# Performance work log

Hardware: AMD Instinct MI355X
Metric: run time of the kernel (lower is better)

Reference implementation:

```python
import jax, jax.numpy as jnp
import numpy as np
import math

B, NLAT, DIM = 16, 64, 768
DEPTH, HEADS, DH = 6, 16, 64
INNER = HEADS * DH          # 1024
FF = 4 * DIM                # 3072
FR_DIMS = [64, 128, 256, 512]
LENS = [3136, 784, 196, 49]  # 56^2, 28^2, 14^2, 7^2 backbone stages
EPS = 1e-5


def layernorm(x, w, b):
    m = jnp.mean(x, axis=-1, keepdims=True)
    v = jnp.mean((x - m) ** 2, axis=-1, keepdims=True)
    return (x - m) * jax.lax.rsqrt(v + EPS) * w + b


def perceiver_attn(x, latents, ln1w, ln1b, ln2w, ln2b, wq, wkv, wo):
    # x: (b, n1, D) image features; latents: (b, n2, D)
    xn = layernorm(x, ln1w, ln1b)
    ln_lat = layernorm(latents, ln2w, ln2b)
    b, l, _ = ln_lat.shape
    q = ln_lat @ wq                                   # (b, n2, H*Dh)
    kv = jnp.concatenate([xn, ln_lat], axis=1) @ wkv  # (b, n1+n2, 2*H*Dh)
    k, v = jnp.split(kv, 2, axis=-1)
    def to_heads(t):
        return t.reshape(b, t.shape[1], HEADS, DH).transpose(0, 2, 1, 3)
    q, k, v = to_heads(q), to_heads(k), to_heads(v)   # (b, h, n, Dh)
    scale = 1.0 / math.sqrt(math.sqrt(DH))            # double-sqrt scaling
    w = jnp.einsum('bhqd,bhkd->bhqk', q * scale, k * scale)
    w = jax.nn.softmax(w.astype(jnp.float32), axis=-1).astype(q.dtype)
    out = jnp.einsum('bhqk,bhkd->bhqd', w, v)
    out = out.transpose(0, 2, 1, 3).reshape(b, l, INNER)
    return out @ wo


def setup_inputs() -> dict:
    key = jax.random.key(0)
    ks = iter(jax.random.split(key, 48))
    nrm = lambda shape, s=0.02: (jax.random.normal(next(ks), shape, jnp.float32) * s)
    inp = {
        'id_embedding': jax.random.normal(next(ks), (B, NLAT, DIM), jnp.float32),
        'f0': jax.random.normal(next(ks), (B, LENS[0], FR_DIMS[0]), jnp.float32),
        'f1': jax.random.normal(next(ks), (B, LENS[1], FR_DIMS[1]), jnp.float32),
        'f2': jax.random.normal(next(ks), (B, LENS[2], FR_DIMS[2]), jnp.float32),
        'f3': jax.random.normal(next(ks), (B, LENS[3], FR_DIMS[3]), jnp.float32),
        # per-scale input projections (Linear with bias)
        'p0_w': nrm((FR_DIMS[0], DIM)), 'p0_b': jnp.zeros((DIM,), jnp.float32),
        'p1_w': nrm((FR_DIMS[1], DIM)), 'p1_b': jnp.zeros((DIM,), jnp.float32),
        'p2_w': nrm((FR_DIMS[2], DIM)), 'p2_b': jnp.zeros((DIM,), jnp.float32),
        'p3_w': nrm((FR_DIMS[3], DIM)), 'p3_b': jnp.zeros((DIM,), jnp.float32),
        # stacked PerceiverAttention params: (depth, 4 scales, ...)
        'attn_ln1_w': jnp.ones((DEPTH, 4, DIM), jnp.float32),
        'attn_ln1_b': jnp.zeros((DEPTH, 4, DIM), jnp.float32),
        'attn_ln2_w': jnp.ones((DEPTH, 4, DIM), jnp.float32),
        'attn_ln2_b': jnp.zeros((DEPTH, 4, DIM), jnp.float32),
        'attn_wq': nrm((DEPTH, 4, DIM, INNER)),
        'attn_wkv': nrm((DEPTH, 4, DIM, 2 * INNER)),
        'attn_wo': nrm((DEPTH, 4, INNER, DIM)),
        # stacked FeedForward params: (depth, ...)
        'ff_ln_w': jnp.ones((DEPTH, DIM), jnp.float32),
        'ff_ln_b': jnp.zeros((DEPTH, DIM), jnp.float32),
        'ff_w1': nrm((DEPTH, DIM, FF)),
        'ff_w2': nrm((DEPTH, FF, DIM)),
        # output head (zero-init in source; randomized here for a nontrivial baseline)
        'proj_out_w': nrm((DIM, DIM)),
        'proj_out_b': jnp.zeros((DIM,), jnp.float32),
        'norm_out_w': jnp.ones((DIM,), jnp.float32),
        'norm_out_b': jnp.zeros((DIM,), jnp.float32),
    }
    return inp


def reference(id_embedding, f0, f1, f2, f3,
              p0_w, p0_b, p1_w, p1_b, p2_w, p2_b, p3_w, p3_b,
              attn_ln1_w, attn_ln1_b, attn_ln2_w, attn_ln2_b,
              attn_wq, attn_wkv, attn_wo,
              ff_ln_w, ff_ln_b, ff_w1, ff_w2,
              proj_out_w, proj_out_b, norm_out_w, norm_out_b):
    # source projects in reversed order: feats[0] <- deepest stage (f3)
    feats = [f3 @ p3_w + p3_b,
             f2 @ p2_w + p2_b,
             f1 @ p1_w + p1_b,
             f0 @ p0_w + p0_b]
    lat = id_embedding
    for d in range(DEPTH):
        for i in range(4):
            lat = perceiver_attn(feats[i], lat,
                                 attn_ln1_w[d, i], attn_ln1_b[d, i],
                                 attn_ln2_w[d, i], attn_ln2_b[d, i],
                                 attn_wq[d, i], attn_wkv[d, i], attn_wo[d, i]) + lat
        h = layernorm(lat, ff_ln_w[d], ff_ln_b[d])
        lat = jax.nn.gelu(h @ ff_w1[d], approximate=False) @ ff_w2[d] + lat
    out = lat @ proj_out_w + proj_out_b
    return layernorm(out, norm_out_w, norm_out_b)
```

## Files before the change

### kernel.cpp

```cpp
#include <hip/hip_runtime.h>
#include <hip/hip_bf16.h>
#include <cstdint>
#include <cstddef>

typedef __hip_bfloat16 bf16;
typedef float  f32x4   __attribute__((ext_vector_type(4)));
typedef float  float4v __attribute__((ext_vector_type(4)));
typedef short  short8  __attribute__((ext_vector_type(8)));
typedef short  short4v __attribute__((ext_vector_type(4)));
typedef __bf16 bf16x8  __attribute__((ext_vector_type(8)));

__device__ __forceinline__ void mfma16(f32x4& d, short8 a, short8 b) {
  d = __builtin_amdgcn_mfma_f32_16x16x32_bf16(
      __builtin_bit_cast(bf16x8, a), __builtin_bit_cast(bf16x8, b), d, 0, 0, 0);
}
__device__ __forceinline__ unsigned short f2b_bits(float x) {
  __hip_bfloat16 h = __float2bfloat16(x);
  return __builtin_bit_cast(unsigned short, h);
}
__device__ __forceinline__ float gelu_exact(float x) {
  return 0.5f * x * (1.0f + erff(x * 0.7071067811865475f));
}

__global__ __launch_bounds__(256) void k_cvt(const float* __restrict__ src,
                                             bf16* __restrict__ dst, int n4) {
  int i = blockIdx.x * 256 + threadIdx.x;
  if (i >= n4) return;
  float4v v = *(const float4v*)(src + (size_t)i * 4);
  short4v s;
  s[0] = (short)f2b_bits(v[0]); s[1] = (short)f2b_bits(v[1]);
  s[2] = (short)f2b_bits(v[2]); s[3] = (short)f2b_bits(v[3]);
  *(short4v*)((short*)dst + (size_t)i * 4) = s;
}

template <bool DUAL>
__global__ __launch_bounds__(256) void k_tfoldx(const float* __restrict__ src,
                                                const float* __restrict__ s1,
                                                const float* __restrict__ s2,
                                                bf16* __restrict__ d1,
                                                bf16* __restrict__ d2,
                                                int K, int N,
                                                long long src_bs, long long s_bs,
                                                long long d1_bs, long long d2_bs) {
  src += (size_t)blockIdx.z * src_bs;
  d1  += (size_t)blockIdx.z * d1_bs;
  if (DUAL) d2 += (size_t)blockIdx.z * d2_bs;
  __shared__ float tile[64][65];
  __shared__ float sc1[64], sc2[64];
  const int n0 = blockIdx.x * 64, k0 = blockIdx.y * 64;
  const int t = threadIdx.x;
  if (t < 64) {
    sc1[t] = s1 ? (s1 + (size_t)blockIdx.z * s_bs)[k0 + t] : 1.0f;
  } else if (DUAL && t < 128) {
    sc2[t - 64] = (s2 + (size_t)blockIdx.z * s_bs)[k0 + t - 64];
  }
#pragma unroll
  for (int j = 0; j < 4; ++j) {
    int f = t + j * 256;
    int row = f >> 4, col = (f & 15) * 4;
    float4v v = *(const float4v*)(src + (size_t)(k0 + row) * N + n0 + col);
    tile[row][col]     = v[0];
    tile[row][col + 1] = v[1];
    tile[row][col + 2] = v[2];
    tile[row][col + 3] = v[3];
  }
  __syncthreads();
#pragma unroll
  for (int j = 0; j < 2; ++j) {
    int s = t + j * 256;
    int n = s >> 3, kc = (s & 7) * 8;
    short8 o1v, o2v;
#pragma unroll
    for (int i = 0; i < 8; ++i) {
      float v = tile[kc + i][n];
      o1v[i] = (short)f2b_bits(v * sc1[kc + i]);
      if (DUAL) o2v[i] = (short)f2b_bits(v * sc2[kc + i]);
    }
    *(short8*)(d1 + (size_t)(n0 + n) * K + k0 + kc) = o1v;
    if (DUAL) *(short8*)(d2 + (size_t)(n0 + n) * K + k0 + kc) = o2v;
  }
}

__global__ __launch_bounds__(256) void k_bfoldv(const float* __restrict__ W,
                                                const float* __restrict__ lnb,
                                                float* __restrict__ out, int K, int N,
                                                long long w_bs, long long b_bs, long long o_bs) {
  W   += (size_t)blockIdx.y * w_bs;
  lnb += (size_t)blockIdx.y * b_bs;
  out += (size_t)blockIdx.y * o_bs;
  __shared__ float sb[768];
  for (int k = threadIdx.x; k < K; k += 256) sb[k] = lnb[k];
  __syncthreads();
  const int lane = threadIdx.x & 63, kg = threadIdx.x >> 6;
  const int n = blockIdx.x * 256 + lane * 4;
  float4v a = {0.f, 0.f, 0.f, 0.f};
  for (int k = kg; k < K; k += 4) {
    float4v wv = *(const float4v*)(W + (size_t)k * N + n);
    float c = sb[k];
    a[0] = fmaf(c, wv[0], a[0]); a[1] = fmaf(c, wv[1], a[1]);
    a[2] = fmaf(c, wv[2], a[2]); a[3] = fmaf(c, wv[3], a[3]);
  }
  __shared__ float4v red[4][64];
  red[kg][lane] = a;
  __syncthreads();
  if (kg == 0) {
    float4v r = red[0][lane] + red[1][lane] + red[2][lane] + red[3][lane];
    *(float4v*)(out + n) = r;
  }
}

__global__ __launch_bounds__(256) void k_kvfold(const float* __restrict__ wkv,
                                                const float* __restrict__ ln2b,
                                                const float* __restrict__ ln1b,
                                                const float* __restrict__ ln1w,
                                                const float* __restrict__ b0,
                                                const float* __restrict__ b1,
                                                const float* __restrict__ b2,
                                                const float* __restrict__ b3,
                                                float* __restrict__ pbuf) {
  const int di = blockIdx.y;
  const int kz = blockIdx.z;
  const int i = di & 3;
  const float* pb = (i == 0) ? b0 : (i == 1) ? b1 : (i == 2) ? b2 : b3;
  const float* W = wkv + (size_t)di * 768 * 2048;
  __shared__ float c2b[96], c1b[96], c1w[96], cpw[96];
  if (threadIdx.x < 96) {
    int k = kz * 96 + threadIdx.x;
    float w1 = ln1w[(size_t)di * 768 + k];
    c2b[threadIdx.x] = ln2b[(size_t)di * 768 + k];
    c1b[threadIdx.x] = ln1b[(size_t)di * 768 + k];
    c1w[threadIdx.x] = w1;
    cpw[threadIdx.x] = pb[k] * w1;
  }
  __syncthreads();
  const int lane = threadIdx.x & 63, kg = threadIdx.x >> 6;
  const int n = blockIdx.x * 256 + lane * 4;
  float4v a1 = {0.f,0.f,0.f,0.f}, a2 = a1, a3 = a1, a4 = a1;
  for (int kk = kg; kk < 96; kk += 4) {
    float4v wv = *(const float4v*)(W + (size_t)(kz * 96 + kk) * 2048 + n);
    float s1 = c2b[kk], s2 = c1b[kk], s3 = c1w[kk], s4 = cpw[kk];
#pragma unroll
    for (int q = 0; q < 4; ++q) {
      a1[q] = fmaf(s1, wv[q], a1[q]);
      a2[q] = fmaf(s2, wv[q], a2[q]);
      a3[q] = fmaf(s3, wv[q], a3[q]);
      a4[q] = fmaf(s4, wv[q], a4[q]);
    }
  }
  __shared__ float4v red[4][64];
  red[kg][lane] = a1; __syncthreads();
  if (kg == 0) {
    float4v r = red[0][lane] + red[1][lane] + red[2][lane] + red[3][lane];
    *(float4v*)(pbuf + (((size_t)0 * 8 + kz) * 24 + di) * 2048 + n) = r;
  }
  __syncthreads();
  red[kg][lane] = a2; __syncthreads();
  if (kg == 0) {
    float4v r = red[0][lane] + red[1][lane] + red[2][lane] + red[3][lane];
    *(float4v*)(pbuf + (((size_t)1 * 8 + kz) * 24 + di) * 2048 + n) = r;
  }
  __syncthreads();
  red[kg][lane] = a3; __syncthreads();
  if (kg == 0) {
    float4v r = red[0][lane] + red[1][lane] + red[2][lane] + red[3][lane];
    *(float4v*)(pbuf + (((size_t)2 * 8 + kz) * 24 + di) * 2048 + n) = r;
  }
  __syncthreads();
  red[kg][lane] = a4; __syncthreads();
  if (kg == 0) {
    float4v r = red[0][lane] + red[1][lane] + red[2][lane] + red[3][lane];
    *(float4v*)(pbuf + (((size_t)3 * 8 + kz) * 24 + di) * 2048 + n) = r;
  }
}

__global__ __launch_bounds__(256) void k_kvred(const float* __restrict__ pbuf,
                                               float* __restrict__ qb,
                                               float* __restrict__ kb,
                                               float* __restrict__ sv,
                                               float* __restrict__ bw) {
  const int di = blockIdx.y;
  const int n = blockIdx.x * 256 + threadIdx.x;
  float a0 = 0.f, a1 = 0.f, a2 = 0.f, a3 = 0.f;
  for (int kz = 0; kz < 8; ++kz) {
    a0 += pbuf[(((size_t)0 * 8 + kz) * 24 + di) * 2048 + n];
    a1 += pbuf[(((size_t)1 * 8 + kz) * 24 + di) * 2048 + n];
    a2 += pbuf[(((size_t)2 * 8 + kz) * 24 + di) * 2048 + n];
    a3 += pbuf[(((size_t)3 * 8 + kz) * 24 + di) * 2048 + n];
  }
  qb[(size_t)di * 3072 + 1024 + n] = a0;
  kb[(size_t)di * 2048 + n] = a1;
  sv[(size_t)di * 2048 + n] = a2;
  bw[(size_t)di * 2048 + n] = a3;
}

__global__ __launch_bounds__(256) void k_std(const float* __restrict__ src,
                                             bf16* __restrict__ dst) {
  int row = blockIdx.x;
  const float* x = src + (size_t)row * 768;
  int t = threadIdx.x;
  float a0 = x[t], a1 = x[t + 256], a2 = x[t + 512];
  float s = a0 + a1 + a2;
  float q = a0 * a0 + a1 * a1 + a2 * a2;
#pragma unroll
  for (int off = 1; off < 64; off <<= 1) { s += __shfl_xor(s, off); q += __shfl_xor(q, off); }
  __shared__ float ss[4], qs[4];
  if ((t & 63) == 0) { ss[t >> 6] = s; qs[t >> 6] = q; }
  __syncthreads();
  s = ss[0] + ss[1] + ss[2] + ss[3];
  q = qs[0] + qs[1] + qs[2] + qs[3];
  float mean = s * (1.0f / 768.0f);
  float var  = q * (1.0f / 768.0f) - mean * mean;
  float inv  = rsqrtf(var + 1e-5f);
  bf16* d = dst + (size_t)row * 768;
  d[t]       = __float2bfloat16((a0 - mean) * inv);
  d[t + 256] = __float2bfloat16((a1 - mean) * inv);
  d[t + 512] = __float2bfloat16((a2 - mean) * inv);
}

__global__ __launch_bounds__(256) void k_stats(const float* __restrict__ src,
                                               float2* __restrict__ out) {
  int row = blockIdx.x;
  const float* x = src + (size_t)row * 768;
  int t = threadIdx.x;
  float a0 = x[t], a1 = x[t + 256], a2 = x[t + 512];
  float s = a0 + a1 + a2;
  float q = a0 * a0 + a1 * a1 + a2 * a2;
#pragma unroll
  for (int off = 1; off < 64; off <<= 1) { s += __shfl_xor(s, off); q += __shfl_xor(q, off); }
  __shared__ float ss[4], qs[4];
  if ((t & 63) == 0) { ss[t >> 6] = s; qs[t >> 6] = q; }
  __syncthreads();
  if (t == 0) {
    float sm = ss[0] + ss[1] + ss[2] + ss[3];
    float qm = qs[0] + qs[1] + qs[2] + qs[3];
    float mean = sm * (1.0f / 768.0f);
    float var  = qm * (1.0f / 768.0f) - mean * mean;
    float inv  = rsqrtf(var + 1e-5f);
    out[row] = make_float2(inv, mean * inv);
  }
}

__global__ __launch_bounds__(256) void k_lnout(const float* __restrict__ src,
                                               const float* __restrict__ w,
                                               const float* __restrict__ b,
                                               float* __restrict__ dst) {
  int row = blockIdx.x;
  const float* x = src + (size_t)row * 768;
  int t = threadIdx.x;
  float a0 = x[t], a1 = x[t + 256], a2 = x[t + 512];
  float s = a0 + a1 + a2;
  float q = a0 * a0 + a1 * a1 + a2 * a2;
#pragma unroll
  for (int off = 1; off < 64; off <<= 1) { s += __shfl_xor(s, off); q += __shfl_xor(q, off); }
  __shared__ float ss[4], qs[4];
  if ((t & 63) == 0) { ss[t >> 6] = s; qs[t >> 6] = q; }
  __syncthreads();
  s = ss[0] + ss[1] + ss[2] + ss[3];
  q = qs[0] + qs[1] + qs[2] + qs[3];
  float mean = s * (1.0f / 768.0f);
  float var  = q * (1.0f / 768.0f) - mean * mean;
  float inv  = rsqrtf(var + 1e-5f);
  float* d = dst + (size_t)row * 768;
  d[t]       = (a0 - mean) * inv * w[t]       + b[t];
  d[t + 256] = (a1 - mean) * inv * w[t + 256] + b[t + 256];
  d[t + 512] = (a2 - mean) * inv * w[t + 512] + b[t + 512];
}

template <int BM, int BN, bool OBF16, bool GELU, bool KVE>
__global__ __launch_bounds__(256) void k_gemm(const bf16* __restrict__ A,
                                              const bf16* __restrict__ Bt,
                                              void* __restrict__ Cv,
                                              const float* __restrict__ bias,
                                              const float* __restrict__ res,
                                              const float2* __restrict__ rstats,
                                              const float* __restrict__ c1,
                                              const float* __restrict__ cs,
                                              int M, int N, int K, int nxt, int nwg) {
  constexpr int AI = BM / 32, BI = BN / 32;
  constexpr int MF = BM / 32, NF = BN / 32;
  __shared__ __align__(16) char smem[(BM + BN) * 128];
  char* As = smem;
  char* Bs = smem + BM * 128;

  const int lin = blockIdx.x;
  const int qq = nwg >> 3, r8 = nwg & 7;
  const int xcd = lin & 7, idx = lin >> 3;
  const int swz = (xcd < r8) ? (xcd * (qq + 1) + idx)
                             : (r8 * (qq + 1) + (xcd - r8) * qq + idx);
  const int bm = (swz / nxt) * BM, bn = (swz % nxt) * BN;

  const int t = threadIdx.x, lane = t & 63, w = t >> 6;
  const int wr = w >> 1, wc = w & 1;
  const int l15 = lane & 15, lg = lane >> 4;
  const int srow = t >> 3, scol = t & 7;

  const bf16* aptr[AI]; int aoff[AI];
#pragma unroll
  for (int i = 0; i < AI; ++i) {
    int r = i * 32 + srow;
    int gr = bm + r; if (gr > M - 1) gr = M - 1;
    aptr[i] = A + (size_t)gr * K + scol * 8;
    aoff[i] = r * 128 + ((scol * 16) ^ ((r & 7) << 4));
  }
  const bf16* bptr[BI]; int boff[BI];
#pragma unroll
  for (int i = 0; i < BI; ++i) {
    int r = i * 32 + srow;
    int gc = bn + r; if (gc > N - 1) gc = N - 1;
    bptr[i] = Bt + (size_t)gc * K + scol * 8;
    boff[i] = r * 128 + ((scol * 16) ^ ((r & 7) << 4));
  }

  f32x4 acc[MF][NF] = {};
  short8 av[AI], bv[BI];
#pragma unroll
  for (int i = 0; i < AI; ++i) av[i] = *(const short8*)(aptr[i]);
#pragma unroll
  for (int i = 0; i < BI; ++i) bv[i] = *(const short8*)(bptr[i]);

  const int nk = K / 64;
  for (int kt = 0; kt < nk; ++kt) {
    __syncthreads();
#pragma unroll
    for (int i = 0; i < AI; ++i) *(short8*)(As + aoff[i]) = av[i];
#pragma unroll
    for (int i = 0; i < BI; ++i) *(short8*)(Bs + boff[i]) = bv[i];
    __syncthreads();
    if (kt + 1 < nk) {
#pragma unroll
      for (int i = 0; i < AI; ++i) av[i] = *(const short8*)(aptr[i] + (size_t)(kt + 1) * 64);
#pragma unroll
      for (int i = 0; i < BI; ++i) bv[i] = *(const short8*)(bptr[i] + (size_t)(kt + 1) * 64);
    }
#pragma unroll
    for (int ks = 0; ks < 2; ++ks) {
      short8 af[MF], bfr[NF];
#pragma unroll
      for (int m = 0; m < MF; ++m) {
        int r = wr * (BM / 2) + m * 16 + l15;
        af[m] = *(const short8*)(As + r * 128 + ((ks * 64 + lg * 16) ^ ((r & 7) << 4)));
      }
#pragma unroll
      for (int n = 0; n < NF; ++n) {
        int r = wc * (BN / 2) + n * 16 + l15;
        bfr[n] = *(const short8*)(Bs + r * 128 + ((ks * 64 + lg * 16) ^ ((r & 7) << 4)));
      }
#pragma unroll
      for (int m = 0; m < MF; ++m)
#pragma unroll
        for (int n = 0; n < NF; ++n) mfma16(acc[m][n], af[m], bfr[n]);
    }
  }

  if (OBF16) {
    __syncthreads();
    bf16* cst = (bf16*)smem;
#pragma unroll
    for (int m = 0; m < MF; ++m) {
      int lr0 = wr * (BM / 2) + m * 16 + lg * 4;
#pragma unroll
      for (int n = 0; n < NF; ++n) {
        int lc = wc * (BN / 2) + n * 16 + l15;
        int gc = bn + lc;
        float bvs = bias ? bias[gc] : 0.0f;
        float c1v = 0.0f, csv = 0.0f;
        if (KVE) { c1v = c1[gc]; csv = cs[gc]; }
#pragma unroll
        for (int r = 0; r < 4; ++r) {
          int row = lr0 + r;
          float v;
          if (KVE) {
            int gri = bm + row; if (gri > M - 1) gri = M - 1;
            float2 st = rstats[gri];
            v = (acc[m][n][r] + c1v) * st.x - st.y * csv + bvs;
          } else {
            v = acc[m][n][r] + bvs;
            if (GELU) v = gelu_exact(v);
          }
          cst[row * BN + lc] = __float2bfloat16(v);
        }
      }
    }
    __syncthreads();
    constexpr int CB = BN / 8;
    constexpr int SEGS = BM * CB;
    for (int seg = t; seg < SEGS; seg += 256) {
      int row = seg / CB, cb = seg % CB;
      int gr = bm + row;
      if (gr < M)
        *(short8*)((bf16*)Cv + (size_t)gr * N + bn + cb * 8) =
            *(const short8*)(cst + (size_t)row * BN + cb * 8);
    }
  } else {
#pragma unroll
    for (int m = 0; m < MF; ++m) {
      int gr0 = bm + wr * (BM / 2) + m * 16 + lg * 4;
#pragma unroll
      for (int n = 0; n < NF; ++n) {
        int gc = bn + wc * (BN / 2) + n * 16 + l15;
        float bvs = bias ? bias[gc] : 0.0f;
#pragma unroll
        for (int r = 0; r < 4; ++r) {
          int gr = gr0 + r;
          if (gr < M) {
            float v = acc[m][n][r] + bvs;
            if (GELU) v = gelu_exact(v);
            if (res) v += res[(size_t)gr * N + gc];
            ((float*)Cv)[(size_t)gr * N + gc] = v;
          }
        }
      }
    }
  }
}

template <bool FUSED>
__global__ __launch_bounds__(256) void k_attn(const bf16* __restrict__ qkvl,
                                              const bf16* __restrict__ kvx,
                                              bf16* __restrict__ outp,
                                              float* __restrict__ opart,
                                              float* __restrict__ mlpart,
                                              int n1, int b0, int nseg, int nbloc,
                                              const bf16* __restrict__ fsrc,
                                              const bf16* __restrict__ PT,
                                              const float2* __restrict__ rst,
                                              const float* __restrict__ c1vec,
                                              const float* __restrict__ csvec,
                                              const float* __restrict__ lbvec) {
  const int s   = blockIdx.x % nseg;
  const int bh  = blockIdx.x / nseg;
  const int bl = bh >> 4, h = bh & 15;
  const int b = b0 + bl;
  const int nb64 = nbloc * 64;
  __shared__ __align__(16) char Qs[64 * 128];
  __shared__ __align__(16) char Ks[64 * 128];
  __shared__ __align__(16) char Vt[64 * 128];
  __shared__ __align__(16) char Ps[4][16 * 128];
  __shared__ __align__(16) char Fs[FUSED ? 64 * 128 : 16];
  __shared__ __align__(16) char PTks[FUSED ? 64 * 128 : 16];
  __shared__ __align__(16) char PTvs[FUSED ? 64 * 128 : 16];
  __shared__ float2 Rs[FUSED ? 64 : 1];
  const int t = threadIdx.x, lane = t & 63, w = t >> 6;
  const int l15 = lane & 15, lg = lane >> 4;

#pragma unroll
  for (int it = 0; it < 2; ++it) {
    int slot = it * 256 + t; int r = slot >> 3, c = slot & 7;
    short8 v = *(const short8*)(qkvl + (size_t)(b * 64 + r) * 3072 + h * 64 + c * 8);
    *(short8*)(Qs + r * 128 + ((c * 16) ^ ((r & 7) << 4))) = v;
  }
  float c1k[4], csk[4], lbk[4], c1v_[4], csv_[4], lbv_[4];
  if constexpr (FUSED) {
#pragma unroll
    for (int it = 0; it < 2; ++it) {
      int slot = it * 256 + t; int r = slot >> 3, c = slot & 7;
      *(short8*)(PTks + r * 128 + ((c * 16) ^ ((r & 7) << 4))) =
          *(const short8*)(PT + (size_t)(h * 64 + r) * 64 + c * 8);
      *(short8*)(PTvs + r * 128 + ((c * 16) ^ ((r & 7) << 4))) =
          *(const short8*)(PT + (size_t)(1024 + h * 64 + r) * 64 + c * 8);
    }
#pragma unroll
    for (int n = 0; n < 4; ++n) {
      int dk = h * 64 + n * 16 + l15;
      c1k[n] = c1vec[dk]; csk[n] = csvec[dk]; lbk[n] = lbvec[dk];
      int dv = 1024 + dk;
      c1v_[n] = c1vec[dv]; csv_[n] = csvec[dv]; lbv_[n] = lbvec[dv];
    }
  }
  const int n_kv = n1 + 64;
  const int nch = (n_kv + 63) >> 6;
  const int cpseg = (nch + nseg - 1) / nseg;
  const int ch0 = s * cpseg;
  const int ch1 = min(nch, ch0 + cpseg);

  float m_run = -1e30f, l_run = 0.0f;
  f32x4 o[4] = {};

  short8 kreg[2], vreg[2], freg[2];
  float2 rreg = make_float2(0.f, 0.f);
  auto loadKV = [&](int ch) {
#pragma unroll
    for (int it = 0; it < 2; ++it) {
      int slot = it * 256 + t; int rr = slot >> 3, c = slot & 7;
      int j = ch * 64 + rr;
      short8 kv = {}; short8 vv = {};
      if (j < n_kv) {
        const bf16* kb;
        if (j < n1) kb = kvx + (size_t)(bl * n1 + j) * 2048 + h * 64;
        else        kb = qkvl + (size_t)(b * 64 + (j - n1)) * 3072 + 1024 + h * 64;
        kv = *(const short8*)(kb + c * 8);
        vv = *(const short8*)(kb + 1024 + c * 8);
      }
      kreg[it] = kv; vreg[it] = vv;
    }
  };
  auto loadF = [&](int ch) {
#pragma unroll
    for (int it = 0; it < 2; ++it) {
      int slot = it * 256 + t; int rr = slot >> 3, c = slot & 7;
      freg[it] = *(const short8*)(fsrc + ((size_t)b * n1 + (size_t)ch * 64 + rr) * 64 + c * 8);
    }
    if (t < 64) rreg = rst[(size_t)b * n1 + (size_t)ch * 64 + t];
  };
  auto isLat = [&](int ch) { return ch * 64 >= n1; };

  if (FUSED && !isLat(ch0)) loadF(ch0); else loadKV(ch0);

  for (int ch = ch0; ch < ch1; ++ch) {
    const bool lat = !FUSED || isLat(ch);
    __syncthreads();
    if (lat) {
#pragma unroll
      for (int it = 0; it < 2; ++it) {
        int slot = it * 256 + t; int rr = slot >> 3, c = slot & 7;
        *(short8*)(Ks + rr * 128 + ((c * 16) ^ ((rr & 7) << 4))) = kreg[it];
#pragma unroll
        for (int j2 = 0; j2 < 8; ++j2) {
          int dh = c * 8 + j2;
          *(short*)(Vt + dh * 128 + ((rr * 2) ^ ((dh & 7) << 4))) = vreg[it][j2];
        }
      }
    } else {
#pragma unroll
      for (int it = 0; it < 2; ++it) {
        int slot = it * 256 + t; int rr = slot >> 3, c = slot & 7;
        *(short8*)(Fs + rr * 128 + ((c * 16) ^ ((rr & 7) << 4))) = freg[it];
      }
      if (t < 64) Rs[t] = rreg;
    }
    __syncthreads();
    if (ch + 1 < ch1) {
      if (FUSED && !isLat(ch + 1)) loadF(ch + 1); else loadKV(ch + 1);
    }
    if constexpr (FUSED) {
      if (!lat) {
        f32x4 ka[4] = {};
#pragma unroll
        for (int ks = 0; ks < 2; ++ks) {
          int fr = w * 16 + l15;
          short8 ff = *(const short8*)(Fs + fr * 128 + ((ks * 64 + lg * 16) ^ ((fr & 7) << 4)));
#pragma unroll
          for (int n = 0; n < 4; ++n) {
            int pr = n * 16 + l15;
            short8 pk = *(const short8*)(PTks + pr * 128 + ((ks * 64 + lg * 16) ^ ((pr & 7) << 4)));
            mfma16(ka[n], ff, pk);
          }
        }
#pragma unroll
        for (int n = 0; n < 4; ++n)
#pragma unroll
          for (int r = 0; r < 4; ++r) {
            int jl = w * 16 + lg * 4 + r;
            float2 st = Rs[jl];
            float v = (ka[n][r] + c1k[n]) * st.x - st.y * csk[n] + lbk[n];
            int dh = n * 16 + l15;
            *(unsigned short*)(Ks + jl * 128 + ((dh * 2) ^ ((jl & 7) << 4))) = f2b_bits(v);
          }
        f32x4 va[4] = {};
#pragma unroll
        for (int ks = 0; ks < 2; ++ks) {
          int fr = w * 16 + l15;
          short8 ff = *(const short8*)(Fs + fr * 128 + ((ks * 64 + lg * 16) ^ ((fr & 7) << 4)));
#pragma unroll
          for (int n = 0; n < 4; ++n) {
            int pr = n * 16 + l15;
            short8 pv = *(const short8*)(PTvs + pr * 128 + ((ks * 64 + lg * 16) ^ ((pr & 7) << 4)));
            mfma16(va[n], ff, pv);
          }
        }
#pragma unroll
        for (int n = 0; n < 4; ++n)
#pragma unroll
          for (int r = 0; r < 4; ++r) {
            int jl = w * 16 + lg * 4 + r;
            float2 st = Rs[jl];
            float v = (va[n][r] + c1v_[n]) * st.x - st.y * csv_[n] + lbv_[n];
            int dh = n * 16 + l15;
            *(unsigned short*)(Vt + dh * 128 + ((jl * 2) ^ ((dh & 7) << 4))) = f2b_bits(v);
          }
      }
      __syncthreads();
    }

    f32x4 sc[4] = {};
#pragma unroll
    for (int ks = 0; ks < 2; ++ks) {
      int qr = w * 16 + l15;
      short8 qf = *(const short8*)(Qs + qr * 128 + ((ks * 64 + lg * 16) ^ ((qr & 7) << 4)));
#pragma unroll
      for (int n = 0; n < 4; ++n) {
        int kr = n * 16 + l15;
        short8 kf = *(const short8*)(Ks + kr * 128 + ((ks * 64 + lg * 16) ^ ((kr & 7) << 4)));
        mfma16(sc[n], kf, qf);
      }
    }
    float mx = m_run;
#pragma unroll
    for (int n = 0; n < 4; ++n)
#pragma unroll
      for (int r = 0; r < 4; ++r) {
        float v = sc[n][r] * 0.125f;
        int kvi = ch * 64 + n * 16 + lg * 4 + r;
        if (kvi >= n_kv) v = -1e30f;
        sc[n][r] = v;
        mx = fmaxf(mx, v);
      }
    mx = fmaxf(mx, __shfl_xor(mx, 16));
    mx = fmaxf(mx, __shfl_xor(mx, 32));
    float scl = __expf(m_run - mx);
    m_run = mx;
    float p[4][4];
    float rs = 0.0f;
#pragma unroll
    for (int n = 0; n < 4; ++n)
#pragma unroll
      for (int r = 0; r < 4; ++r) { float pv = __expf(sc[n][r] - mx); p[n][r] = pv; rs += pv; }
    rs += __shfl_xor(rs, 16);
    rs += __shfl_xor(rs, 32);
    l_run = l_run * scl + rs;
    float sclq[4];
#pragma unroll
    for (int r = 0; r < 4; ++r) sclq[r] = __shfl(scl, lg * 4 + r);
#pragma unroll
    for (int nn = 0; nn < 4; ++nn)
#pragma unroll
      for (int r = 0; r < 4; ++r) o[nn][r] *= sclq[r];
#pragma unroll
    for (int n = 0; n < 4; ++n)
#pragma unroll
      for (int r = 0; r < 4; ++r) {
        int kv = n * 16 + lg * 4 + r;
        *(unsigned short*)(Ps[w] + l15 * 128 + ((kv * 2) ^ ((l15 & 7) << 4))) = f2b_bits(p[n][r]);
      }
#pragma unroll
    for (int ks = 0; ks < 2; ++ks) {
      short8 pf = *(const short8*)(Ps[w] + l15 * 128 + ((ks * 64 + lg * 16) ^ ((l15 & 7) << 4)));
#pragma unroll
      for (int nn = 0; nn < 4; ++nn) {
        int dh = nn * 16 + l15;
        short8 vf = *(const short8*)(Vt + dh * 128 + ((ks * 64 + lg * 16) ^ ((dh & 7) << 4)));
        mfma16(o[nn], pf, vf);
      }
    }
  }

  if (nseg == 1) {
    float lq[4];
#pragma unroll
    for (int r = 0; r < 4; ++r) lq[r] = __shfl(l_run, lg * 4 + r);
#pragma unroll
    for (int nn = 0; nn < 4; ++nn)
#pragma unroll
      for (int r = 0; r < 4; ++r) {
        int qr = w * 16 + lg * 4 + r;
        int dh = nn * 16 + l15;
        outp[(size_t)(b * 64 + qr) * 1024 + h * 64 + dh] = __float2bfloat16(o[nn][r] / lq[r]);
      }
  } else {
#pragma unroll
    for (int nn = 0; nn < 4; ++nn)
#pragma unroll
      for (int r = 0; r < 4; ++r) {
        int qr = w * 16 + lg * 4 + r;
        int dh = nn * 16 + l15;
        opart[((size_t)s * nb64 + bl * 64 + qr) * 1024 + h * 64 + dh] = o[nn][r];
      }
    if (lg == 0) {
      int qr = w * 16 + l15;
      size_t mi = (((size_t)s * nb64 + bl * 64 + qr) * 16 + h) * 2;
      mlpart[mi]     = m_run;
      mlpart[mi + 1] = l_run;
    }
  }
}

__global__ __launch_bounds__(256) void k_amerge(const float* __restrict__ opart,
                                                const float* __restrict__ mlpart,
                                                bf16* __restrict__ outp,
                                                int b0, int nseg, int nbloc) {
  const int bh = blockIdx.x;
  const int bl = bh >> 4, h = bh & 15;
  const int nb64 = nbloc * 64;
  const int t = threadIdx.x;
  const int q = t >> 2, quarter = t & 3;

  float ms[8], ls[8];
  float mstar = -1e30f;
  for (int s = 0; s < nseg; ++s) {
    size_t mi = (((size_t)s * nb64 + bl * 64 + q) * 16 + h) * 2;
    ms[s] = mlpart[mi]; ls[s] = mlpart[mi + 1];
    mstar = fmaxf(mstar, ms[s]);
  }
  float L = 0.0f, ws[8];
  for (int s = 0; s < nseg; ++s) { ws[s] = __expf(ms[s] - mstar); L += ws[s] * ls[s]; }
  float inv = 1.0f / L;

  bf16* outrow = outp + (size_t)((b0 + bl) * 64 + q) * 1024 + h * 64;
#pragma unroll
  for (int jj = 0; jj < 4; ++jj) {
    int dh0 = quarter * 16 + jj * 4;
    float4v acc = {0.f, 0.f, 0.f, 0.f};
    for (int s = 0; s < nseg; ++s) {
      const float* orow = opart + ((size_t)s * nb64 + bl * 64 + q) * 1024 + h * 64 + dh0;
      float4v v = *(const float4v*)orow;
      acc[0] += ws[s] * v[0]; acc[1] += ws[s] * v[1];
      acc[2] += ws[s] * v[2]; acc[3] += ws[s] * v[3];
    }
    short4v sv;
    sv[0] = (short)f2b_bits(acc[0] * inv); sv[1] = (short)f2b_bits(acc[1] * inv);
    sv[2] = (short)f2b_bits(acc[2] * inv); sv[3] = (short)f2b_bits(acc[3] * inv);
    *(short4v*)((short*)(outrow + dh0)) = sv;
  }
}

extern "C" void kernel_launch(void* const* d_in, const int* in_sizes, int n_in,
                              void* d_out, int out_size, void* d_ws, size_t ws_size,
                              hipStream_t stream) {
  (void)in_sizes; (void)n_in; (void)out_size;
  const float* id_emb = (const float*)d_in[0];
  const float* f_in[4]  = {(const float*)d_in[4],  (const float*)d_in[3],
                           (const float*)d_in[2],  (const float*)d_in[1]};
  const float* pw_in[4] = {(const float*)d_in[11], (const float*)d_in[9],
                           (const float*)d_in[7],  (const float*)d_in[5]};
  const float* pb_in[4] = {(const float*)d_in[12], (const float*)d_in[10],
                           (const float*)d_in[8],  (const float*)d_in[6]};
  const float* ln1w = (const float*)d_in[13];
  const float* ln1b = (const float*)d_in[14];
  const float* ln2w = (const float*)d_in[15];
  const float* ln2b = (const float*)d_in[16];
  const float* wq   = (const float*)d_in[17];
  const float* wkv  = (const float*)d_in[18];
  const float* wo   = (const float*)d_in[19];
  const float* fflnw = (const float*)d_in[20];
  const float* fflnb = (const float*)d_in[21];
  const float* ffw1  = (const float*)d_in[22];
  const float* ffw2  = (const float*)d_in[23];
  const float* projw = (const float*)d_in[24];
  const float* projb = (const float*)d_in[25];
  const float* normw = (const float*)d_in[26];
  const float* normb = (const float*)d_in[27];

  static const int N1S[4]  = {49, 196, 784, 3136};
  static const int FRDS[4] = {512, 256, 128, 64};
  static const int NSEG[4] = {1, 1, 2, 4};
  const size_t LW = 4718592;
  static const size_t ROFF[4] = {0, 16*49ull, 16*(49+196ull), 16*(49+196+784ull)};

  bf16 *fbf[4], *pT[4], *pbf[4], *projT, *PTbuf;
  float *qkvl_bias, *kvx_bias, *ff_bias, *lat, *headtmp, *svv, *bwv, *pbuf;
  float2 *rstats;
  float *opart, *mlpart;
  bf16 *qkvl_act, *attnout, *zlat, *latbf, *ffh;
  bf16 *wqkvlT = nullptr, *wkvxT = nullptr, *woT = nullptr, *w1T = nullptr, *w2T = nullptr;
  bf16 *wbuf = nullptr;
  char *big;

  auto assign = [&](bool fullw, int bc) -> size_t {
    size_t off = 0; char* base = (char*)d_ws;
    auto A = [&](size_t b) -> char* {
      char* p = base + off; off = (off + b + 255) & ~(size_t)255; return p;
    };
    for (int i = 0; i < 4; ++i) fbf[i] = (bf16*)A((size_t)16 * N1S[i] * FRDS[i] * 2);
    for (int i = 0; i < 4; ++i) pT[i]  = (bf16*)A((size_t)768 * FRDS[i] * 2);
    for (int i = 0; i < 4; ++i) pbf[i] = (bf16*)A((size_t)FRDS[i] * 768 * 2);
    projT     = (bf16*)A(768ull * 768 * 2);
    PTbuf     = (bf16*)A(2048ull * 512 * 2);
    qkvl_bias = (float*)A(24ull * 3072 * 4);
    kvx_bias  = (float*)A(24ull * 2048 * 4);
    ff_bias   = (float*)A(6ull * 3072 * 4);
    svv       = (float*)A(24ull * 2048 * 4);
    bwv       = (float*)A(24ull * 2048 * 4);
    pbuf      = (float*)A(4ull * 8 * 24 * 2048 * 4);
    rstats    = (float2*)A(16ull * 4165 * 8);
    qkvl_act  = (bf16*)A(1024ull * 3072 * 2);
    attnout   = (bf16*)A(1024ull * 1024 * 2);
    lat       = (float*)A(1024ull * 768 * 4);
    zlat      = (bf16*)A(1024ull * 768 * 2);
    opart     = (float*)A(4ull * (size_t)bc * 64 * 1024 * 4);
    mlpart    = (float*)A(4ull * (size_t)bc * 64 * 16 * 2 * 4);
    if (fullw) {
      wqkvlT = (bf16*)A(24ull * 3072 * 768 * 2);
      wkvxT  = (bf16*)A(24ull * 2048 * 768 * 2);
      woT    = (bf16*)A(24ull * 768 * 1024 * 2);
      w1T    = (bf16*)A(6ull * 3072 * 768 * 2);
      w2T    = (bf16*)A(6ull * 768 * 3072 * 2);
      wbuf = nullptr;
    } else {
      wbuf = (bf16*)A(4ull * LW * 2);
      wqkvlT = wkvxT = woT = w1T = w2T = nullptr;
    }
    big = A((size_t)bc * 3136 * 2048 * 2);
    ffh = qkvl_act; headtmp = (float*)qkvl_act; latbf = zlat;
    return off;
  };

  static const bool FULLS[10] = {true,true,false,true,false,true,true,false,false,false};
  static const int  BCS[10]   = {16,  8,   16,   4,   8,    2,   1,   4,    2,    1};
  bool fullw = false; int bc = 1; bool ok = false;
  for (int c = 0; c < 10; ++c) {
    if (assign(FULLS[c], BCS[c]) <= ws_size) { fullw = FULLS[c]; bc = BCS[c]; ok = true; break; }
  }
  if (!ok) return;

  float* featf32 = (float*)big;
  bf16*  kvxbuf  = (bf16*)big;

  auto gemm = [&](int tile, const bf16* A, const bf16* Bt, void* C,
                  const float* bias, const float* res, int M, int N, int K,
                  bool obf, bool gl) {
    if (tile == 128) {
      int nxt = N / 128, nwg = nxt * ((M + 127) / 128);
      if (obf && gl) k_gemm<128,128,true ,true ,false><<<nwg,256,0,stream>>>(A,Bt,C,bias,res,nullptr,nullptr,nullptr,M,N,K,nxt,nwg);
      else if (obf)  k_gemm<128,128,true ,false,false><<<nwg,256,0,stream>>>(A,Bt,C,bias,res,nullptr,nullptr,nullptr,M,N,K,nxt,nwg);
      else           k_gemm<128,128,false,false,false><<<nwg,256,0,stream>>>(A,Bt,C,bias,res,nullptr,nullptr,nullptr,M,N,K,nxt,nwg);
    } else if (tile == 64) {
      int nxt = N / 64, nwg = nxt * ((M + 63) / 64);
      if (obf && gl)  k_gemm<64,64,true ,true ,false><<<nwg,256,0,stream>>>(A,Bt,C,bias,res,nullptr,nullptr,nullptr,M,N,K,nxt,nwg);
      else if (obf)   k_gemm<64,64,true ,false,false><<<nwg,256,0,stream>>>(A,Bt,C,bias,res,nullptr,nullptr,nullptr,M,N,K,nxt,nwg);
      else            k_gemm<64,64,false,false,false><<<nwg,256,0,stream>>>(A,Bt,C,bias,res,nullptr,nullptr,nullptr,M,N,K,nxt,nwg);
    } else {
      int nxt = N / 64, nwg = nxt * ((M + 31) / 32);
      if (obf && gl)  k_gemm<32,64,true ,true ,false><<<nwg,256,0,stream>>>(A,Bt,C,bias,res,nullptr,nullptr,nullptr,M,N,K,nxt,nwg);
      else if (obf)   k_gemm<32,64,true ,false,false><<<nwg,256,0,stream>>>(A,Bt,C,bias,res,nullptr,nullptr,nullptr,M,N,K,nxt,nwg);
      else            k_gemm<32,64,false,false,false><<<nwg,256,0,stream>>>(A,Bt,C,bias,res,nullptr,nullptr,nullptr,M,N,K,nxt,nwg);
    }
  };
  auto gemmkv = [&](const bf16* A, const bf16* Bt, void* C,
                    const float* lb, const float2* rst, const float* c1, const float* cs,
                    int M, int N, int K) {
    if (M >= 2048) {
      int nxt = N / 128, nwg = nxt * ((M + 127) / 128);
      k_gemm<128,128,true,false,true><<<nwg,256,0,stream>>>(A,Bt,C,lb,nullptr,rst,c1,cs,M,N,K,nxt,nwg);
    } else {
      int nxt = N / 64, nwg = nxt * ((M + 63) / 64);
      k_gemm<64,64,true,false,true><<<nwg,256,0,stream>>>(A,Bt,C,lb,nullptr,rst,c1,cs,M,N,K,nxt,nwg);
    }
  };
  auto pick = [&](int M, int N) -> int {
    return M >= 2048 ? 128 : (N >= 1536 ? 64 : 32);
  };

  k_bfoldv<<<dim3(4, 24), 256, 0, stream>>>(wq,  ln2b, qkvl_bias, 768, 1024, 768LL*1024, 768, 3072);
  k_kvfold<<<dim3(8, 24, 8), 256, 0, stream>>>(wkv, ln2b, ln1b, ln1w,
                                               pb_in[0], pb_in[1], pb_in[2], pb_in[3], pbuf);
  k_kvred<<<dim3(8, 24), 256, 0, stream>>>(pbuf, qkvl_bias, kvx_bias, svv, bwv);
  k_bfoldv<<<dim3(12, 6), 256, 0, stream>>>(ffw1, fflnb, ff_bias, 768, 3072, 768LL*3072, 768, 3072);

  for (int i = 0; i < 4; ++i) {
    k_tfoldx<false><<<dim3(12, FRDS[i] / 64, 1), 256, 0, stream>>>(
        pw_in[i], nullptr, nullptr, pT[i], nullptr, FRDS[i], 768, 0, 0, 0, 0);
    int cnt = FRDS[i] * 768;
    k_cvt<<<cnt / 1024, 256, 0, stream>>>(pw_in[i], pbf[i], cnt / 4);
  }
  k_tfoldx<false><<<dim3(12, 12, 1), 256, 0, stream>>>(
      projw, nullptr, nullptr, projT, nullptr, 768, 768, 0, 0, 0, 0);

  if (fullw) {
    k_tfoldx<false><<<dim3(16, 12, 24), 256, 0, stream>>>(
        wq, ln2w, nullptr, wqkvlT, nullptr, 768, 1024, 768LL*1024, 768, 3072LL*768, 0);
    k_tfoldx<true><<<dim3(32, 12, 24), 256, 0, stream>>>(
        wkv, ln2w, ln1w, wqkvlT + 1024LL*768, wkvxT, 768, 2048,
        768LL*2048, 768, 3072LL*768, 2048LL*768);
    k_tfoldx<false><<<dim3(12, 16, 24), 256, 0, stream>>>(
        wo, nullptr, nullptr, woT, nullptr, 1024, 768, 1024LL*768, 0, 768LL*1024, 0);
    k_tfoldx<false><<<dim3(48, 12, 6), 256, 0, stream>>>(
        ffw1, fflnw, nullptr, w1T, nullptr, 768, 3072, 768LL*3072, 768, 3072LL*768, 0);
    k_tfoldx<false><<<dim3(12, 48, 6), 256, 0, stream>>>(
        ffw2, nullptr, nullptr, w2T, nullptr, 3072, 768, 3072LL*768, 0, 768LL*3072, 0);
  }

  auto foldDepthAttn = [&](int d) {
    k_tfoldx<false><<<dim3(16, 12, 4), 256, 0, stream>>>(
        wq + (size_t)d*4*768*1024, ln2w + (size_t)d*4*768, nullptr,
        wbuf, nullptr, 768, 1024, 768LL*1024, 768, (long long)LW, 0);
    k_tfoldx<true><<<dim3(32, 12, 4), 256, 0, stream>>>(
        wkv + (size_t)d*4*768*2048, ln2w + (size_t)d*4*768, ln1w + (size_t)d*4*768,
        wbuf + 1024ull*768, wbuf + 3072ull*768, 768, 2048,
        768LL*2048, 768, (long long)LW, (long long)LW);
    k_tfoldx<false><<<dim3(12, 16, 4), 256, 0, stream>>>(
        wo + (size_t)d*4*1024*768, nullptr, nullptr,
        wbuf + 3932160ull, nullptr, 1024, 768, 1024LL*768, 0, (long long)LW, 0);
  };
  auto attnW = [&](int di, const bf16*& qkvlT_p, const bf16*& kvxT_p, const bf16*& woT_p) {
    if (fullw) {
      qkvlT_p = wqkvlT + (size_t)di * 3072 * 768;
      kvxT_p  = wkvxT  + (size_t)di * 2048 * 768;
      woT_p   = woT    + (size_t)di * 768 * 1024;
    } else {
      bf16* base = wbuf + (size_t)(di & 3) * LW;
      qkvlT_p = base;
      kvxT_p  = base + 2359296ull;
      woT_p   = base + 3932160ull;
    }
  };
  auto ffW = [&](int d, const bf16*& w1p, const bf16*& w2p) {
    if (fullw) {
      w1p = w1T + (size_t)d * 3072 * 768;
      w2p = w2T + (size_t)d * 768 * 3072;
    } else {
      bf16* d1 = wbuf;
      bf16* d2 = wbuf + 3072ull * 768;
      k_tfoldx<false><<<dim3(48, 12, 1), 256, 0, stream>>>(
          ffw1 + (size_t)d*768*3072, fflnw + 768ull*d, nullptr, d1, nullptr,
          768, 3072, 0, 0, 0, 0);
      k_tfoldx<false><<<dim3(12, 48, 1), 256, 0, stream>>>(
          ffw2 + (size_t)d*3072*768, nullptr, nullptr, d2, nullptr,
          3072, 768, 0, 0, 0, 0);
      w1p = d1; w2p = d2;
    }
  };

  for (int i = 0; i < 4; ++i) {
    int n1 = N1S[i], frd = FRDS[i];
    size_t cnt = (size_t)16 * n1 * frd;
    k_cvt<<<(int)(cnt / 1024), 256, 0, stream>>>(f_in[i], fbf[i], (int)(cnt / 4));
    for (int b0 = 0; b0 < 16; b0 += bc) {
      int rows = bc * n1;
      gemm(pick(rows, 768), fbf[i] + (size_t)b0 * n1 * frd, pT[i], featf32,
           pb_in[i], nullptr, rows, 768, frd, false, false);
      k_stats<<<rows, 256, 0, stream>>>(featf32, rstats + ROFF[i] + (size_t)b0 * n1);
    }
  }

  hipMemcpyAsync(lat, id_emb, 1024ull * 768 * 4, hipMemcpyDeviceToDevice, stream);

  for (int d = 0; d < 6; ++d) {
    if (!fullw) foldDepthAttn(d);
    for (int i = 0; i < 4; ++i) {
      int di = d * 4 + i, n1 = N1S[i], nseg = NSEG[i], frd = FRDS[i];
      const bf16 *qkvlT_p, *kvxT_p, *woT_p;
      attnW(di, qkvlT_p, kvxT_p, woT_p);
      gemm(64, kvxT_p, pbf[i], PTbuf, nullptr, nullptr, 2048, frd, 768, true, false);
      k_std<<<1024, 256, 0, stream>>>(lat, zlat);
      gemm(64, zlat, qkvlT_p, qkvl_act, qkvl_bias + 3072ull * di, nullptr,
           1024, 3072, 768, true, false);
      for (int b0 = 0; b0 < 16; b0 += bc) {
        int rows = bc * n1;
        if (i == 3) {
          k_attn<true><<<bc * 16 * nseg, 256, 0, stream>>>(
              qkvl_act, kvxbuf, attnout, opart, mlpart, n1, b0, nseg, bc,
              fbf[3], PTbuf, rstats + ROFF[3],
              bwv + 2048ull * di, svv + 2048ull * di, kvx_bias + 2048ull * di);
        } else {
          gemmkv(fbf[i] + (size_t)b0 * n1 * frd, PTbuf, kvxbuf,
                 kvx_bias + 2048ull * di, rstats + ROFF[i] + (size_t)b0 * n1,
                 bwv + 2048ull * di, svv + 2048ull * di, rows, 2048, frd);
          k_attn<false><<<bc * 16 * nseg, 256, 0, stream>>>(
              qkvl_act, kvxbuf, attnout, opart, mlpart, n1, b0, nseg, bc,
              nullptr, nullptr, nullptr, nullptr, nullptr, nullptr);
        }
        if (nseg > 1)
          k_amerge<<<bc * 16, 256, 0, stream>>>(opart, mlpart, attnout, b0, nseg, bc);
      }
      gemm(32, attnout, woT_p, lat, nullptr, lat, 1024, 768, 1024, false, false);
    }
    const bf16 *w1p, *w2p;
    ffW(d, w1p, w2p);
    k_std<<<1024, 256, 0, stream>>>(lat, zlat);
    gemm(64, zlat, w1p, ffh, ff_bias + 3072ull * d, nullptr, 1024, 3072, 768, true, true);
    gemm(32, ffh, w2p, lat, nullptr, lat, 1024, 768, 3072, false, false);
  }

  k_cvt<<<768, 256, 0, stream>>>(lat, latbf, 196608);
  gemm(32, latbf, projT, headtmp, projb, nullptr, 1024, 768, 768, false, false);
  k_lnout<<<1024, 256, 0, stream>>>(headtmp, normw, normb, (float*)d_out);
}
```

Measured before the change: 2.951 ms.

## Batch composed KV-projection weight GEMMs upfront and split-K the bias folds

All 24 per-layer products of the KV weight with the input projection weights are now computed before the depth loop. Each scale gets one launch batched over depth through a new blockIdx.y stride in the GEMM kernel, replacing 24 small serialized GEMMs inside the loop. The bias-fold kernels are split along K across 8 z-blocks with a separate reduction kernel, giving more parallelism to what was a tiny grid. This adds workspace for the precomputed products and one extra small launch per bias fold.

```diff
diff --git a/kernel.cpp b/kernel.cpp
--- a/kernel.cpp
+++ b/kernel.cpp
@@ -81,22 +81,22 @@
   }
 }
 
-__global__ __launch_bounds__(256) void k_bfoldv(const float* __restrict__ W,
-                                                const float* __restrict__ lnb,
-                                                float* __restrict__ out, int K, int N,
-                                                long long w_bs, long long b_bs, long long o_bs) {
-  W   += (size_t)blockIdx.y * w_bs;
-  lnb += (size_t)blockIdx.y * b_bs;
-  out += (size_t)blockIdx.y * o_bs;
-  __shared__ float sb[768];
-  for (int k = threadIdx.x; k < K; k += 256) sb[k] = lnb[k];
+__global__ __launch_bounds__(256) void k_bfoldz(const float* __restrict__ W,
+                                                const float* __restrict__ b,
+                                                float* __restrict__ pbuf, int K, int N,
+                                                long long w_bs, long long b_bs) {
+  W += (size_t)blockIdx.y * w_bs;
+  b += (size_t)blockIdx.y * b_bs;
+  const int kz = blockIdx.z, kpz = K >> 3;
+  __shared__ float sb[96];
+  if ((int)threadIdx.x < kpz) sb[threadIdx.x] = b[kz * kpz + threadIdx.x];
   __syncthreads();
   const int lane = threadIdx.x & 63, kg = threadIdx.x >> 6;
   const int n = blockIdx.x * 256 + lane * 4;
   float4v a = {0.f, 0.f, 0.f, 0.f};
-  for (int k = kg; k < K; k += 4) {
-    float4v wv = *(const float4v*)(W + (size_t)k * N + n);
-    float c = sb[k];
+  for (int kk = kg; kk < kpz; kk += 4) {
+    float4v wv = *(const float4v*)(W + (size_t)(kz * kpz + kk) * N + n);
+    float c = sb[kk];
     a[0] = fmaf(c, wv[0], a[0]); a[1] = fmaf(c, wv[1], a[1]);
     a[2] = fmaf(c, wv[2], a[2]); a[3] = fmaf(c, wv[3], a[3]);
   }
@@ -105,8 +105,18 @@
   __syncthreads();
   if (kg == 0) {
     float4v r = red[0][lane] + red[1][lane] + red[2][lane] + red[3][lane];
-    *(float4v*)(out + n) = r;
-  }
+    *(float4v*)(pbuf + ((size_t)kz * gridDim.y + blockIdx.y) * N + n) = r;
+  }
+}
+
+__global__ __launch_bounds__(256) void k_bred(const float* __restrict__ pbuf,
+                                              float* __restrict__ out, int N, int NB,
+                                              long long o_bs) {
+  const int by = blockIdx.y;
+  const int n = blockIdx.x * 256 + threadIdx.x;
+  float a = 0.f;
+  for (int kz = 0; kz < 8; ++kz) a += pbuf[((size_t)kz * NB + by) * N + n];
+  out[(size_t)by * o_bs + n] = a;
 }
 
 __global__ __launch_bounds__(256) void k_kvfold(const float* __restrict__ wkv,
@@ -275,12 +285,17 @@
                                               const float2* __restrict__ rstats,
                                               const float* __restrict__ c1,
                                               const float* __restrict__ cs,
-                                              int M, int N, int K, int nxt, int nwg) {
+                                              int M, int N, int K,
+                                              long long azb, long long czb,
+                                              int nxt, int nwg) {
   constexpr int AI = BM / 32, BI = BN / 32;
   constexpr int MF = BM / 32, NF = BN / 32;
   __shared__ __align__(16) char smem[(BM + BN) * 128];
   char* As = smem;
   char* Bs = smem + BM * 128;
+
+  A  = (const bf16*)((const char*)A + (size_t)blockIdx.y * azb);
+  Cv = (void*)((char*)Cv + (size_t)blockIdx.y * czb);
 
   const int lin = blockIdx.x;
   const int qq = nwg >> 3, r8 = nwg & 7;
@@ -745,9 +760,10 @@
   static const int NSEG[4] = {1, 1, 2, 4};
   const size_t LW = 4718592;
   static const size_t ROFF[4] = {0, 16*49ull, 16*(49+196ull), 16*(49+196+784ull)};
-
-  bf16 *fbf[4], *pT[4], *pbf[4], *projT, *PTbuf;
-  float *qkvl_bias, *kvx_bias, *ff_bias, *lat, *headtmp, *svv, *bwv, *pbuf;
+  static const size_t PTO[4]  = {0, 6ull*2048*512, 6ull*2048*(512+256), 6ull*2048*(512+256+128)};
+
+  bf16 *fbf[4], *pT[4], *pbf[4], *projT, *PTbuf, *PTall;
+  float *qkvl_bias, *kvx_bias, *ff_bias, *lat, *headtmp, *svv, *bwv, *pbuf, *pbuf2;
   float2 *rstats;
   float *opart, *mlpart;
   bf16 *qkvl_act, *attnout, *zlat, *latbf, *ffh;
@@ -771,6 +787,7 @@
     svv       = (float*)A(24ull * 2048 * 4);
     bwv       = (float*)A(24ull * 2048 * 4);
     pbuf      = (float*)A(4ull * 8 * 24 * 2048 * 4);
+    pbuf2     = (float*)A(8ull * 24 * 3072 * 4);
     rstats    = (float2*)A(16ull * 4165 * 8);
     qkvl_act  = (bf16*)A(1024ull * 3072 * 2);
     attnout   = (bf16*)A(1024ull * 1024 * 2);
@@ -784,10 +801,12 @@
       woT    = (bf16*)A(24ull * 768 * 1024 * 2);
       w1T    = (bf16*)A(6ull * 3072 * 768 * 2);
       w2T    = (bf16*)A(6ull * 768 * 3072 * 2);
+      PTall  = (bf16*)A(6ull * 2048 * 960 * 2);
       wbuf = nullptr;
     } else {
       wbuf = (bf16*)A(4ull * LW * 2);
       wqkvlT = wkvxT = woT = w1T = w2T = nullptr;
+      PTall = nullptr;
     }
     big = A((size_t)bc * 3136 * 2048 * 2);
     ffh = qkvl_act; headtmp = (float*)qkvl_act; latbf = zlat;
@@ -810,19 +829,19 @@
                   bool obf, bool gl) {
     if (tile == 128) {
       int nxt = N / 128, nwg = nxt * ((M + 127) / 128);
-      if (obf && gl) k_gemm<128,128,true ,true ,false><<<nwg,256,0,stream>>>(A,Bt,C,bias,res,nullptr,nullptr,nullptr,M,N,K,nxt,nwg);
-      else if (obf)  k_gemm<128,128,true ,false,false><<<nwg,256,0,stream>>>(A,Bt,C,bias,res,nullptr,nullptr,nullptr,M,N,K,nxt,nwg);
-      else           k_gemm<128,128,false,false,false><<<nwg,256,0,stream>>>(A,Bt,C,bias,res,nullptr,nullptr,nullptr,M,N,K,nxt,nwg);
+      if (obf && gl) k_gemm<128,128,true ,true ,false><<<nwg,256,0,stream>>>(A,Bt,C,bias,res,nullptr,nullptr,nullptr,M,N,K,0,0,nxt,nwg);
+      else if (obf)  k_gemm<128,128,true ,false,false><<<nwg,256,0,stream>>>(A,Bt,C,bias,res,nullptr,nullptr,nullptr,M,N,K,0,0,nxt,nwg);
+      else           k_gemm<128,128,false,false,false><<<nwg,256,0,stream>>>(A,Bt,C,bias,res,nullptr,nullptr,nullptr,M,N,K,0,0,nxt,nwg);
     } else if (tile == 64) {
       int nxt = N / 64, nwg = nxt * ((M + 63) / 64);
-      if (obf && gl)  k_gemm<64,64,true ,true ,false><<<nwg,256,0,stream>>>(A,Bt,C,bias,res,nullptr,nullptr,nullptr,M,N,K,nxt,nwg);
-      else if (obf)   k_gemm<64,64,true ,false,false><<<nwg,256,0,stream>>>(A,Bt,C,bias,res,nullptr,nullptr,nullptr,M,N,K,nxt,nwg);
-      else            k_gemm<64,64,false,false,false><<<nwg,256,0,stream>>>(A,Bt,C,bias,res,nullptr,nullptr,nullptr,M,N,K,nxt,nwg);
+      if (obf && gl)  k_gemm<64,64,true ,true ,false><<<nwg,256,0,stream>>>(A,Bt,C,bias,res,nullptr,nullptr,nullptr,M,N,K,0,0,nxt,nwg);
+      else if (obf)   k_gemm<64,64,true ,false,false><<<nwg,256,0,stream>>>(A,Bt,C,bias,res,nullptr,nullptr,nullptr,M,N,K,0,0,nxt,nwg);
+      else            k_gemm<64,64,false,false,false><<<nwg,256,0,stream>>>(A,Bt,C,bias,res,nullptr,nullptr,nullptr,M,N,K,0,0,nxt,nwg);
     } else {
       int nxt = N / 64, nwg = nxt * ((M + 31) / 32);
-      if (obf && gl)  k_gemm<32,64,true ,true ,false><<<nwg,256,0,stream>>>(A,Bt,C,bias,res,nullptr,nullptr,nullptr,M,N,K,nxt,nwg);
-      else if (obf)   k_gemm<32,64,true ,false,false><<<nwg,256,0,stream>>>(A,Bt,C,bias,res,nullptr,nullptr,nullptr,M,N,K,nxt,nwg);
-      else            k_gemm<32,64,false,false,false><<<nwg,256,0,stream>>>(A,Bt,C,bias,res,nullptr,nullptr,nullptr,M,N,K,nxt,nwg);
+      if (obf && gl)  k_gemm<32,64,true ,true ,false><<<nwg,256,0,stream>>>(A,Bt,C,bias,res,nullptr,nullptr,nullptr,M,N,K,0,0,nxt,nwg);
+      else if (obf)   k_gemm<32,64,true ,false,false><<<nwg,256,0,stream>>>(A,Bt,C,bias,res,nullptr,nullptr,nullptr,M,N,K,0,0,nxt,nwg);
+      else            k_gemm<32,64,false,false,false><<<nwg,256,0,stream>>>(A,Bt,C,bias,res,nullptr,nullptr,nullptr,M,N,K,0,0,nxt,nwg);
     }
   };
   auto gemmkv = [&](const bf16* A, const bf16* Bt, void* C,
@@ -830,21 +849,23 @@
                     int M, int N, int K) {
     if (M >= 2048) {
       int nxt = N / 128, nwg = nxt * ((M + 127) / 128);
-      k_gemm<128,128,true,false,true><<<nwg,256,0,stream>>>(A,Bt,C,lb,nullptr,rst,c1,cs,M,N,K,nxt,nwg);
+      k_gemm<128,128,true,false,true><<<nwg,256,0,stream>>>(A,Bt,C,lb,nullptr,rst,c1,cs,M,N,K,0,0,nxt,nwg);
     } else {
       int nxt = N / 64, nwg = nxt * ((M + 63) / 64);
-      k_gemm<64,64,true,false,true><<<nwg,256,0,stream>>>(A,Bt,C,lb,nullptr,rst,c1,cs,M,N,K,nxt,nwg);
+      k_gemm<64,64,true,false,true><<<nwg,256,0,stream>>>(A,Bt,C,lb,nullptr,rst,c1,cs,M,N,K,0,0,nxt,nwg);
     }
   };
   auto pick = [&](int M, int N) -> int {
     return M >= 2048 ? 128 : (N >= 1536 ? 64 : 32);
   };
 
-  k_bfoldv<<<dim3(4, 24), 256, 0, stream>>>(wq,  ln2b, qkvl_bias, 768, 1024, 768LL*1024, 768, 3072);
+  k_bfoldz<<<dim3(4, 24, 8), 256, 0, stream>>>(wq, ln2b, pbuf2, 768, 1024, 768LL*1024, 768);
+  k_bred  <<<dim3(4, 24), 256, 0, stream>>>(pbuf2, qkvl_bias, 1024, 24, 3072);
   k_kvfold<<<dim3(8, 24, 8), 256, 0, stream>>>(wkv, ln2b, ln1b, ln1w,
                                                pb_in[0], pb_in[1], pb_in[2], pb_in[3], pbuf);
-  k_kvred<<<dim3(8, 24), 256, 0, stream>>>(pbuf, qkvl_bias, kvx_bias, svv, bwv);
-  k_bfoldv<<<dim3(12, 6), 256, 0, stream>>>(ffw1, fflnb, ff_bias, 768, 3072, 768LL*3072, 768, 3072);
+  k_kvred <<<dim3(8, 24), 256, 0, stream>>>(pbuf, qkvl_bias, kvx_bias, svv, bwv);
+  k_bfoldz<<<dim3(12, 6, 8), 256, 0, stream>>>(ffw1, fflnb, pbuf2, 768, 3072, 768LL*3072, 768);
+  k_bred  <<<dim3(12, 6), 256, 0, stream>>>(pbuf2, ff_bias, 3072, 6, 3072);
 
   for (int i = 0; i < 4; ++i) {
     k_tfoldx<false><<<dim3(12, FRDS[i] / 64, 1), 256, 0, stream>>>(
@@ -867,6 +888,14 @@
         ffw1, fflnw, nullptr, w1T, nullptr, 768, 3072, 768LL*3072, 768, 3072LL*768, 0);
     k_tfoldx<false><<<dim3(12, 48, 6), 256, 0, stream>>>(
         ffw2, nullptr, nullptr, w2T, nullptr, 3072, 768, 3072LL*768, 0, 768LL*3072, 0);
+    for (int i = 0; i < 4; ++i) {
+      int frd = FRDS[i];
+      int nxt = frd / 64, nwg = nxt * 32;
+      k_gemm<64,64,true,false,false><<<dim3(nwg, 6), 256, 0, stream>>>(
+          wkvxT + (size_t)i * 2048 * 768, pbf[i], PTall + PTO[i],
+          nullptr, nullptr, nullptr, nullptr, nullptr, 2048, frd, 768,
+          4LL * 2048 * 768 * 2, (long long)2048 * frd * 2, nxt, nwg);
+    }
   }
 
   auto foldDepthAttn = [&](int d) {
@@ -930,7 +959,13 @@
       int di = d * 4 + i, n1 = N1S[i], nseg = NSEG[i], frd = FRDS[i];
       const bf16 *qkvlT_p, *kvxT_p, *woT_p;
       attnW(di, qkvlT_p, kvxT_p, woT_p);
-      gemm(64, kvxT_p, pbf[i], PTbuf, nullptr, nullptr, 2048, frd, 768, true, false);
+      const bf16* PTp;
+      if (fullw) {
+        PTp = PTall + PTO[i] + (size_t)d * 2048 * frd;
+      } else {
+        gemm(64, kvxT_p, pbf[i], PTbuf, nullptr, nullptr, 2048, frd, 768, true, false);
+        PTp = PTbuf;
+      }
       k_std<<<1024, 256, 0, stream>>>(lat, zlat);
       gemm(64, zlat, qkvlT_p, qkvl_act, qkvl_bias + 3072ull * di, nullptr,
            1024, 3072, 768, true, false);
@@ -939,10 +974,10 @@
         if (i == 3) {
           k_attn<true><<<bc * 16 * nseg, 256, 0, stream>>>(
               qkvl_act, kvxbuf, attnout, opart, mlpart, n1, b0, nseg, bc,
-              fbf[3], PTbuf, rstats + ROFF[3],
+              fbf[3], PTp, rstats + ROFF[3],
               bwv + 2048ull * di, svv + 2048ull * di, kvx_bias + 2048ull * di);
         } else {
-          gemmkv(fbf[i] + (size_t)b0 * n1 * frd, PTbuf, kvxbuf,
+          gemmkv(fbf[i] + (size_t)b0 * n1 * frd, PTp, kvxbuf,
                  kvx_bias + 2048ull * di, rstats + ROFF[i] + (size_t)b0 * n1,
                  bwv + 2048ull * di, svv + 2048ull * di, rows, 2048, frd);
           k_attn<false><<<bc * 16 * nseg, 256, 0, stream>>>(
```

Measured after the change: 2.632 ms. 10.8% less time.
